# Kernel optimization log

Measured on AMD Instinct MI355X. Metric: run time of the kernel, lower is better.

## Reference

```python
import jax, jax.numpy as jnp
import numpy as np
import math

B, T, C = 4, 2048, 768
H = 12
D = C // H  # head dim 64

def setup_inputs() -> dict:
    key = jax.random.key(0)
    ks = jax.random.split(key, 7)
    hidden_states = jax.random.normal(ks[0], (B, T, C), dtype=jnp.float32)
    attention_mask = jnp.ones((B, T), dtype=jnp.float32)
    # torch nn.Linear weights are [out, in]; y = x @ W.T + b
    s = 1.0 / math.sqrt(C)
    Wq = jax.random.uniform(ks[1], (C, C), jnp.float32, -s, s)
    bq = jax.random.uniform(ks[2], (C,), jnp.float32, -s, s)
    Wk = jax.random.uniform(ks[3], (C, C), jnp.float32, -s, s)
    bk = jax.random.uniform(ks[4], (C,), jnp.float32, -s, s)
    Wv = jax.random.uniform(ks[5], (C, C), jnp.float32, -s, s)
    bv = jax.random.uniform(ks[6], (C,), jnp.float32, -s, s)
    return {"hidden_states": hidden_states, "attention_mask": attention_mask,
            "Wq": Wq, "bq": bq, "Wk": Wk, "bk": bk, "Wv": Wv, "bv": bv}

def _split_heads(x):
    # [B,T,C] -> [B,H,T,D]
    b, t, c = x.shape
    return x.reshape(b, t, H, D).transpose(0, 2, 1, 3)

def reference(hidden_states, attention_mask, Wq, bq, Wk, bk, Wv, bv):
    q = _split_heads(hidden_states @ Wq.T + bq)
    k = _split_heads(hidden_states @ Wk.T + bk)
    v = _split_heads(hidden_states @ Wv.T + bv)
    scores = jnp.einsum("bhqd,bhkd->bhqk", q, k) / jnp.sqrt(jnp.float32(D))
    # mask: [B,T] -> additive bias [B,1,1,T]
    bias = (1.0 - attention_mask)[:, None, None, :] * -10000.0
    scores = scores + bias
    probs = jax.nn.softmax(scores, axis=-1)  # dropout prob = 0 -> identity
    ctx = jnp.einsum("bhqk,bhkd->bhqd", probs, v)
    # [B,H,T,D] -> [B,T,C]
    return ctx.transpose(0, 2, 1, 3).reshape(hidden_states.shape[0], hidden_states.shape[1], C)
```

## Files before the change

### kernel.cpp

```cpp
#include <hip/hip_runtime.h>
#include <hip/hip_bf16.h>
#include <cstdint>

#define DI __device__ __forceinline__

constexpr int Bz = 4, Tz = 2048, Cz = 768, Hz = 12, Dz = 64;
constexpr float QSCALE = 0.18033688011112042f;

typedef __attribute__((ext_vector_type(4))) float f32x4;
typedef __attribute__((ext_vector_type(16))) float f32x16;
typedef __attribute__((ext_vector_type(8))) __bf16 bf16x8;
typedef __attribute__((ext_vector_type(4))) __bf16 bf16x4;
typedef __attribute__((ext_vector_type(2))) __bf16 bf16x2;

typedef __attribute__((address_space(1))) void gvoid;
typedef __attribute__((address_space(3))) void lvoid;

DI void gload16(const void* g, void* l) {
  __builtin_amdgcn_global_load_lds((gvoid*)g, (lvoid*)l, 16, 0, 0);
}

DI f32x4 mfma16(bf16x8 a, bf16x8 b, f32x4 c) {
  return __builtin_amdgcn_mfma_f32_16x16x32_bf16(a, b, c, 0, 0, 0);
}
DI f32x16 mfma32(bf16x8 a, bf16x8 b, f32x16 c) {
  return __builtin_amdgcn_mfma_f32_32x32x16_bf16(a, b, c, 0, 0, 0);
}

DI uint32_t pk2(float a, float b) {
  bf16x2 t;
  t[0] = (__bf16)a;
  t[1] = (__bf16)b;
  return __builtin_bit_cast(uint32_t, t);
}

union FragU { bf16x8 v; uint32_t u[4]; };

__global__ void cvt_all_k(const float* __restrict__ x,
                          const float* __restrict__ wq, const float* __restrict__ wk,
                          const float* __restrict__ wv, __bf16* __restrict__ Xb,
                          __bf16* __restrict__ Wb) {
  int i = blockIdx.x * blockDim.x + threadIdx.x;
  const float* s;
  __bf16* d;
  int r;
  if (i < 1572864) {
    s = x; d = Xb; r = i;
  } else {
    int j = i - 1572864;
    const int which = j / 147456;
    r = j - which * 147456;
    s = (which == 0) ? wq : (which == 1) ? wk : wv;
    d = Wb + which * 589824 * 2;
    d = Wb + which * 589824;
  }
  const float4 v = reinterpret_cast<const float4*>(s)[r];
  bf16x4 o = {(__bf16)v.x, (__bf16)v.y, (__bf16)v.z, (__bf16)v.w};
  reinterpret_cast<bf16x4*>(d)[r] = o;
}

__global__ __launch_bounds__(256, 4) void qkv_gemm_k(
    const __bf16* __restrict__ Xb, const __bf16* __restrict__ Wb,
    const float* __restrict__ bq, const float* __restrict__ bk,
    const float* __restrict__ bv, __bf16* __restrict__ Qo,
    __bf16* __restrict__ Ko, __bf16* __restrict__ Vo) {
  __shared__ __align__(16) __bf16 As[128 * 64];
  __shared__ __align__(16) __bf16 Bs[128 * 64];

  const int tid = threadIdx.x;
  const int lane = tid & 63;
  const int w = tid >> 6;
  const int wr = w >> 1, wc = w & 1;
  const int g = lane >> 4, lr = lane & 15;

  const int wgid = (blockIdx.x & 7) * 144 + (blockIdx.x >> 3);
  const int tn = wgid % 18, tm = wgid / 18;
  const int m0 = tm * 128, n0 = tn * 128;

  f32x4 acc[4][4] = {};

  for (int kt = 0; kt < Cz; kt += 64) {
#pragma unroll
    for (int rep = 0; rep < 4; ++rep) {
      const int c = rep * 256 + tid;
      const int row = c >> 3, blk = c & 7;
      const int col = ((blk ^ (row & 7)) << 3);
      gload16(&Xb[(size_t)(m0 + row) * Cz + kt + col], &As[c << 3]);
      gload16(&Wb[(size_t)(n0 + row) * Cz + kt + col], &Bs[c << 3]);
    }
    __syncthreads();
#pragma unroll
    for (int kk = 0; kk < 2; ++kk) {
      bf16x8 a[4], b[4];
#pragma unroll
      for (int m = 0; m < 4; ++m) {
        const int row = wr * 64 + m * 16 + lr;
        a[m] = *reinterpret_cast<const bf16x8*>(
            &As[row * 64 + (((kk * 4 + g) ^ (row & 7)) << 3)]);
      }
#pragma unroll
      for (int n = 0; n < 4; ++n) {
        const int row = wc * 64 + n * 16 + lr;
        b[n] = *reinterpret_cast<const bf16x8*>(
            &Bs[row * 64 + (((kk * 4 + g) ^ (row & 7)) << 3)]);
      }
      __builtin_amdgcn_s_setprio(1);
#pragma unroll
      for (int m = 0; m < 4; ++m)
#pragma unroll
        for (int n = 0; n < 4; ++n) acc[m][n] = mfma16(a[m], b[n], acc[m][n]);
      __builtin_amdgcn_s_setprio(0);
    }
    __syncthreads();
  }

  const int bb = m0 >> 11;
  const int tbase = m0 & 2047;
  if (tn >= 12) {
#pragma unroll
    for (int n = 0; n < 4; ++n) {
      const int cc = (n0 - 1536) + wc * 64 + n * 16 + lr;
      const int h = cc >> 6, d = cc & 63;
      const float bsv = bv[cc];
      const int bh = bb * Hz + h;
#pragma unroll
      for (int m = 0; m < 4; ++m) {
        const int tloc = tbase + wr * 64 + m * 16 + g * 4;
        const int k16 = tloc >> 4;
        bf16x4 pkv;
#pragma unroll
        for (int j = 0; j < 4; ++j) pkv[j] = (__bf16)(acc[m][n][j] + bsv);
        *reinterpret_cast<bf16x4*>(
            &Vo[((size_t)(bh * 128 + k16) * 64 + d) * 16 + (tloc & 15)]) = pkv;
      }
    }
  } else {
    const bool isQ = (tn < 6);
#pragma unroll
    for (int n = 0; n < 4; ++n) {
      const int gn = n0 + wc * 64 + n * 16 + lr;
      const int cc = isQ ? gn : (gn - 768);
      const int h = cc >> 6, d = cc & 63;
      const float bsv = isQ ? bq[cc] : bk[cc];
      __bf16* dst = isQ ? Qo : Ko;
      const int bh = bb * Hz + h;
#pragma unroll
      for (int m = 0; m < 4; ++m) {
#pragma unroll
        for (int j = 0; j < 4; ++j) {
          const int t = tbase + wr * 64 + m * 16 + g * 4 + j;
          float v = acc[m][n][j] + bsv;
          if (isQ) v *= QSCALE;
          dst[(size_t)(bh * Tz + t) * Dz + d] = (__bf16)v;
        }
      }
    }
  }
}

__global__ __launch_bounds__(256, 3) void attn_k(
    const __bf16* __restrict__ Qg, const __bf16* __restrict__ Kg,
    const __bf16* __restrict__ Vc, const float* __restrict__ mask,
    float* __restrict__ out) {
  __shared__ __align__(16) __bf16 Ks[2][4096];

  const int tid = threadIdx.x;
  const int lane = tid & 63;
  const int w = tid >> 6;
  const int hi = lane >> 5;
  const int l31 = lane & 31;

  const int wg = (blockIdx.x & 7) * 96 + (blockIdx.x >> 3);
  const int bh = wg >> 4, qt = wg & 15;
  const int bb = bh / Hz, h = bh - bb * Hz;
  const int q0 = qt * 128 + w * 32;

  const size_t qkbase = (size_t)bh * Tz * Dz;
  const size_t vcb = (size_t)bh * Tz * Dz;
  const float* maskp = &mask[bb * Tz];

  int* flag = (int*)&Ks[1][0];
  if (tid == 0) *flag = 0;
  __syncthreads();
  {
    int mybad = 0;
    for (int i = tid; i < Tz; i += 256) mybad |= (maskp[i] != 1.0f);
    if (__any(mybad) && lane == 0) atomicOr(flag, 1);
  }

#pragma unroll
  for (int rep = 0; rep < 2; ++rep) {
    const int c = rep * 256 + tid;
    const int row = c >> 3, blk = c & 7;
    const int col = ((blk ^ (row & 7)) << 3);
    gload16(&Kg[qkbase + (size_t)row * Dz + col], &Ks[0][c << 3]);
  }

  bf16x8 qB[4];
#pragma unroll
  for (int ks = 0; ks < 4; ++ks)
    qB[ks] = *reinterpret_cast<const bf16x8*>(
        &Qg[qkbase + (size_t)(q0 + l31) * Dz + ks * 16 + hi * 8]);

  __syncthreads();
  const bool use_mask = (*flag != 0);

  int off4[4];
#pragma unroll
  for (int i = 0; i < 4; ++i)
    off4[i] = l31 * 64 + (((i * 2 + hi) ^ (l31 & 7)) << 3);

  const int vlane0 = l31 * 16 + hi * 8;

  f32x16 o0 = {}, o1 = {};
  float lpart = 0.f;

  for (int t2 = 0; t2 < 16; ++t2) {
#pragma unroll
    for (int sub = 0; sub < 2; ++sub) {
      const int t = 2 * t2 + sub;
      __syncthreads();

      bf16x8 vB[4][2];
#pragma unroll
      for (int ps4 = 0; ps4 < 4; ++ps4) {
        const size_t cb = vcb + (size_t)(t * 4 + ps4) * 1024;
        vB[ps4][0] = *reinterpret_cast<const bf16x8*>(&Vc[cb + vlane0]);
        vB[ps4][1] = *reinterpret_cast<const bf16x8*>(&Vc[cb + 512 + vlane0]);
      }

      if (t < 31) {
        const int kt1 = (t + 1) * 64;
#pragma unroll
        for (int rep = 0; rep < 2; ++rep) {
          const int c = rep * 256 + tid;
          const int row = c >> 3, blk = c & 7;
          const int col = ((blk ^ (row & 7)) << 3);
          gload16(&Kg[qkbase + (size_t)(kt1 + row) * Dz + col],
                  &Ks[sub ^ 1][c << 3]);
        }
      }
      const int kt = t * 64;

#pragma unroll
      for (int kblk = 0; kblk < 2; ++kblk) {
        bf16x8 kA[4];
#pragma unroll
        for (int ks = 0; ks < 4; ++ks)
          kA[ks] = *reinterpret_cast<const bf16x8*>(
              &Ks[sub][kblk * 2048 + off4[ks]]);

        f32x16 s = {};
        __builtin_amdgcn_s_setprio(1);
#pragma unroll
        for (int ks = 0; ks < 4; ++ks) s = mfma32(kA[ks], qB[ks], s);
        __builtin_amdgcn_s_setprio(0);

        float p[16];
        if (use_mask) {
#pragma unroll
          for (int r = 0; r < 16; ++r) {
            const int kg = kt + kblk * 32 + (r & 3) + 8 * (r >> 2) + 4 * hi;
            p[r] = __builtin_amdgcn_exp2f(
                s[r] + (1.0f - maskp[kg]) * -14426.950408889634f);
            lpart += p[r];
          }
        } else {
#pragma unroll
          for (int r = 0; r < 16; ++r) {
            p[r] = __builtin_amdgcn_exp2f(s[r]);
            lpart += p[r];
          }
        }

        uint32_t a0 = pk2(p[0], p[1]), a1 = pk2(p[4], p[5]);
        uint32_t a2 = pk2(p[8], p[9]), a3 = pk2(p[12], p[13]);
        uint32_t b0 = pk2(p[2], p[3]), b1 = pk2(p[6], p[7]);
        uint32_t b2 = pk2(p[10], p[11]), b3 = pk2(p[14], p[15]);
        asm volatile("v_permlane32_swap_b32 %0, %1" : "+v"(a0), "+v"(a1));
        asm volatile("v_permlane32_swap_b32 %0, %1" : "+v"(b0), "+v"(b1));
        asm volatile("v_permlane32_swap_b32 %0, %1" : "+v"(a2), "+v"(a3));
        asm volatile("v_permlane32_swap_b32 %0, %1" : "+v"(b2), "+v"(b3));
        FragU pf0, pf1;
        pf0.u[0] = a0; pf0.u[1] = b0; pf0.u[2] = a1; pf0.u[3] = b1;
        pf1.u[0] = a2; pf1.u[1] = b2; pf1.u[2] = a3; pf1.u[3] = b3;

        __builtin_amdgcn_s_setprio(1);
        o0 = mfma32(pf0.v, vB[kblk * 2][0], o0);
        o1 = mfma32(pf0.v, vB[kblk * 2][1], o1);
        o0 = mfma32(pf1.v, vB[kblk * 2 + 1][0], o0);
        o1 = mfma32(pf1.v, vB[kblk * 2 + 1][1], o1);
        __builtin_amdgcn_s_setprio(0);
      }
    }
  }

  float lfin = lpart + __shfl_xor(lpart, 32);
  const float inv = 1.0f / lfin;
#pragma unroll
  for (int r = 0; r < 16; ++r) {
    const int qr = (r & 3) + 8 * (r >> 2) + 4 * hi;
    const float invr = __shfl(inv, qr);
    float* orow = &out[(size_t)(bb * Tz + q0 + qr) * Cz + h * Dz + l31];
    orow[0] = o0[r] * invr;
    orow[32] = o1[r] * invr;
  }
}

extern "C" void kernel_launch(void* const* d_in, const int* in_sizes, int n_in,
                              void* d_out, int out_size, void* d_ws,
                              size_t ws_size, hipStream_t stream) {
  const float* x = (const float*)d_in[0];
  const float* mask = (const float*)d_in[1];
  const float* Wq = (const float*)d_in[2];
  const float* bq = (const float*)d_in[3];
  const float* Wk = (const float*)d_in[4];
  const float* bk = (const float*)d_in[5];
  const float* Wv = (const float*)d_in[6];
  const float* bv = (const float*)d_in[7];
  float* out = (float*)d_out;

  char* ws = (char*)d_ws;
  __bf16* Xb = (__bf16*)ws;
  __bf16* Wb = (__bf16*)(ws + 12582912);
  __bf16* Qb = (__bf16*)(ws + 16131072);
  __bf16* Kb = (__bf16*)(ws + 16131072 + 12582912);
  __bf16* Vb = (__bf16*)(ws + 16131072 + 2 * 12582912);

  cvt_all_k<<<7872, 256, 0, stream>>>(x, Wq, Wk, Wv, Xb, Wb);
  qkv_gemm_k<<<1152, 256, 0, stream>>>(Xb, Wb, bq, bk, bv, Qb, Kb, Vb);
  attn_k<<<768, 256, 0, stream>>>(Qb, Kb, Vb, mask, out);
}
```

Measured before the change: 116.4 us.

## Split attention key range across two wave groups with LDS reduction

Each attention workgroup now has 512 threads, with two groups of four waves. Each group processes half of the key sequence for the same 128 query rows, and the partial outputs and row sums are combined through LDS at the end. The goal is to double wave-level parallelism and halve the serial key loop per wave, hiding more latency. In exchange it needs more LDS for the doubled K buffers, extra barriers and a reduction step. It also changes the K swizzle pattern, splits the row-sum accumulator into two to shorten the dependency chain, and removes a dead store in the convert kernel.

```diff
diff --git a/kernel.cpp b/kernel.cpp
--- a/kernel.cpp
+++ b/kernel.cpp
@@ -35,6 +35,8 @@
 }
 
 union FragU { bf16x8 v; uint32_t u[4]; };
+
+DI int kswz(int row) { return (row & 7) ^ (((row >> 3) & 3) << 1); }
 
 __global__ void cvt_all_k(const float* __restrict__ x,
                           const float* __restrict__ wq, const float* __restrict__ wk,
@@ -51,7 +53,6 @@
     const int which = j / 147456;
     r = j - which * 147456;
     s = (which == 0) ? wq : (which == 1) ? wk : wv;
-    d = Wb + which * 589824 * 2;
     d = Wb + which * 589824;
   }
   const float4 v = reinterpret_cast<const float4*>(s)[r];
@@ -158,42 +159,44 @@
   }
 }
 
-__global__ __launch_bounds__(256, 3) void attn_k(
+__global__ __launch_bounds__(512, 6) void attn_k(
     const __bf16* __restrict__ Qg, const __bf16* __restrict__ Kg,
     const __bf16* __restrict__ Vc, const float* __restrict__ mask,
     float* __restrict__ out) {
-  __shared__ __align__(16) __bf16 Ks[2][4096];
+  __shared__ __align__(16) __bf16 KsAll[2][2][4096];
+  __shared__ int flag;
 
   const int tid = threadIdx.x;
   const int lane = tid & 63;
   const int w = tid >> 6;
+  const int w4 = w & 3;
+  const int gw = w >> 2;
   const int hi = lane >> 5;
   const int l31 = lane & 31;
 
   const int wg = (blockIdx.x & 7) * 96 + (blockIdx.x >> 3);
   const int bh = wg >> 4, qt = wg & 15;
   const int bb = bh / Hz, h = bh - bb * Hz;
-  const int q0 = qt * 128 + w * 32;
+  const int q0 = qt * 128 + w4 * 32;
+  const int kb0 = gw * 1024;
 
   const size_t qkbase = (size_t)bh * Tz * Dz;
-  const size_t vcb = (size_t)bh * Tz * Dz;
   const float* maskp = &mask[bb * Tz];
 
-  int* flag = (int*)&Ks[1][0];
-  if (tid == 0) *flag = 0;
+  if (tid == 0) flag = 0;
   __syncthreads();
   {
     int mybad = 0;
-    for (int i = tid; i < Tz; i += 256) mybad |= (maskp[i] != 1.0f);
-    if (__any(mybad) && lane == 0) atomicOr(flag, 1);
-  }
-
-#pragma unroll
-  for (int rep = 0; rep < 2; ++rep) {
-    const int c = rep * 256 + tid;
+    for (int i = tid; i < Tz; i += 512) mybad |= (maskp[i] != 1.0f);
+    if (__any(mybad) && lane == 0) atomicOr(&flag, 1);
+  }
+
+  {
+    const int c = tid;
     const int row = c >> 3, blk = c & 7;
-    const int col = ((blk ^ (row & 7)) << 3);
-    gload16(&Kg[qkbase + (size_t)row * Dz + col], &Ks[0][c << 3]);
+    const int col = ((blk ^ kswz(row)) << 3);
+    gload16(&Kg[qkbase + (size_t)row * Dz + col], &KsAll[0][0][c << 3]);
+    gload16(&Kg[qkbase + (size_t)(1024 + row) * Dz + col], &KsAll[1][0][c << 3]);
   }
 
   bf16x8 qB[4];
@@ -203,19 +206,22 @@
         &Qg[qkbase + (size_t)(q0 + l31) * Dz + ks * 16 + hi * 8]);
 
   __syncthreads();
-  const bool use_mask = (*flag != 0);
-
+  const bool use_mask = (flag != 0);
+
+  const int f31 = (l31 & 7) ^ (((l31 >> 3) & 3) << 1);
+  const __bf16* ksBase = &KsAll[gw][0][0];
   int off4[4];
 #pragma unroll
   for (int i = 0; i < 4; ++i)
-    off4[i] = l31 * 64 + (((i * 2 + hi) ^ (l31 & 7)) << 3);
+    off4[i] = l31 * 64 + (((i * 2 + hi) ^ f31) << 3);
 
   const int vlane0 = l31 * 16 + hi * 8;
+  const size_t vcb0 = qkbase + (size_t)kb0 * Dz;
 
   f32x16 o0 = {}, o1 = {};
-  float lpart = 0.f;
-
-  for (int t2 = 0; t2 < 16; ++t2) {
+  float lpA = 0.f, lpB = 0.f;
+
+  for (int t2 = 0; t2 < 8; ++t2) {
 #pragma unroll
     for (int sub = 0; sub < 2; ++sub) {
       const int t = 2 * t2 + sub;
@@ -224,23 +230,22 @@
       bf16x8 vB[4][2];
 #pragma unroll
       for (int ps4 = 0; ps4 < 4; ++ps4) {
-        const size_t cb = vcb + (size_t)(t * 4 + ps4) * 1024;
+        const size_t cb = vcb0 + (size_t)(t * 4 + ps4) * 1024;
         vB[ps4][0] = *reinterpret_cast<const bf16x8*>(&Vc[cb + vlane0]);
         vB[ps4][1] = *reinterpret_cast<const bf16x8*>(&Vc[cb + 512 + vlane0]);
       }
 
-      if (t < 31) {
+      if (t < 15) {
         const int kt1 = (t + 1) * 64;
-#pragma unroll
-        for (int rep = 0; rep < 2; ++rep) {
-          const int c = rep * 256 + tid;
-          const int row = c >> 3, blk = c & 7;
-          const int col = ((blk ^ (row & 7)) << 3);
-          gload16(&Kg[qkbase + (size_t)(kt1 + row) * Dz + col],
-                  &Ks[sub ^ 1][c << 3]);
-        }
-      }
-      const int kt = t * 64;
+        const int c = tid;
+        const int row = c >> 3, blk = c & 7;
+        const int col = ((blk ^ kswz(row)) << 3);
+        gload16(&Kg[qkbase + (size_t)(kt1 + row) * Dz + col],
+                &KsAll[0][sub ^ 1][c << 3]);
+        gload16(&Kg[qkbase + (size_t)(1024 + kt1 + row) * Dz + col],
+                &KsAll[1][sub ^ 1][c << 3]);
+      }
+      const int kt = kb0 + t * 64;
 
 #pragma unroll
       for (int kblk = 0; kblk < 2; ++kblk) {
@@ -248,7 +253,7 @@
 #pragma unroll
         for (int ks = 0; ks < 4; ++ks)
           kA[ks] = *reinterpret_cast<const bf16x8*>(
-              &Ks[sub][kblk * 2048 + off4[ks]]);
+              &ksBase[sub * 4096 + kblk * 2048 + off4[ks]]);
 
         f32x16 s = {};
         __builtin_amdgcn_s_setprio(1);
@@ -263,13 +268,13 @@
             const int kg = kt + kblk * 32 + (r & 3) + 8 * (r >> 2) + 4 * hi;
             p[r] = __builtin_amdgcn_exp2f(
                 s[r] + (1.0f - maskp[kg]) * -14426.950408889634f);
-            lpart += p[r];
+            ((r & 1) ? lpB : lpA) += p[r];
           }
         } else {
 #pragma unroll
           for (int r = 0; r < 16; ++r) {
             p[r] = __builtin_amdgcn_exp2f(s[r]);
-            lpart += p[r];
+            ((r & 1) ? lpB : lpA) += p[r];
           }
         }
 
@@ -295,15 +300,38 @@
     }
   }
 
-  float lfin = lpart + __shfl_xor(lpart, 32);
-  const float inv = 1.0f / lfin;
-#pragma unroll
-  for (int r = 0; r < 16; ++r) {
-    const int qr = (r & 3) + 8 * (r >> 2) + 4 * hi;
-    const float invr = __shfl(inv, qr);
-    float* orow = &out[(size_t)(bb * Tz + q0 + qr) * Cz + h * Dz + l31];
-    orow[0] = o0[r] * invr;
-    orow[32] = o1[r] * invr;
+  float* cb = (float*)&KsAll[0][0][0];
+  float lp = lpA + lpB;
+  __syncthreads();
+  if (gw == 1)
+#pragma unroll
+    for (int j = 0; j < 16; ++j) cb[w4 * 1024 + lane * 16 + j] = o0[j];
+  __syncthreads();
+  if (gw == 0)
+#pragma unroll
+    for (int j = 0; j < 16; ++j) o0[j] += cb[w4 * 1024 + lane * 16 + j];
+  __syncthreads();
+  if (gw == 1) {
+#pragma unroll
+    for (int j = 0; j < 16; ++j) cb[w4 * 1024 + lane * 16 + j] = o1[j];
+    cb[4096 + w4 * 64 + lane] = lp;
+  }
+  __syncthreads();
+  if (gw == 0) {
+#pragma unroll
+    for (int j = 0; j < 16; ++j) o1[j] += cb[w4 * 1024 + lane * 16 + j];
+    lp += cb[4096 + w4 * 64 + lane];
+
+    float lfin = lp + __shfl_xor(lp, 32);
+    const float inv = 1.0f / lfin;
+#pragma unroll
+    for (int r = 0; r < 16; ++r) {
+      const int qr = (r & 3) + 8 * (r >> 2) + 4 * hi;
+      const float invr = __shfl(inv, qr);
+      float* orow = &out[(size_t)(bb * Tz + q0 + qr) * Cz + h * Dz + l31];
+      orow[0] = o0[r] * invr;
+      orow[32] = o1[r] * invr;
+    }
   }
 }
 
@@ -329,5 +357,5 @@
 
   cvt_all_k<<<7872, 256, 0, stream>>>(x, Wq, Wk, Wv, Xb, Wb);
   qkv_gemm_k<<<1152, 256, 0, stream>>>(Xb, Wb, bq, bk, bv, Qb, Kb, Vb);
-  attn_k<<<768, 256, 0, stream>>>(Qb, Kb, Vb, mask, out);
-}
+  attn_k<<<768, 512, 0, stream>>>(Qb, Kb, Vb, mask, out);
+}
```

Measured after the change: 446.1 us. 283% more time.

## Deepen K prefetch to four LDS buffers with partial waitcnt barrier

Applied to the files above, without the earlier changes.

Makes the attention kernel's K staging a 4-slot LDS ring with prefetch distance two, so each global_load_lds has more time to land. In the unmasked path it replaces the full __syncthreads with s_waitcnt vmcnt(2) plus a raw barrier, so the newest prefetch can stay in flight. It also templates the loop on the mask flag, splits the row-sum into two accumulators, and raises launch bounds to 4 waves/SIMD. The hand-written vmcnt assumes a fixed count of outstanding vector loads per iteration; if the compiler reorders loads, the sync could be wrong.

```diff
diff --git a/kernel.cpp b/kernel.cpp
--- a/kernel.cpp
+++ b/kernel.cpp
@@ -51,7 +51,6 @@
     const int which = j / 147456;
     r = j - which * 147456;
     s = (which == 0) ? wq : (which == 1) ? wk : wv;
-    d = Wb + which * 589824 * 2;
     d = Wb + which * 589824;
   }
   const float4 v = reinterpret_cast<const float4*>(s)[r];
@@ -158,87 +157,33 @@
   }
 }
 
-__global__ __launch_bounds__(256, 3) void attn_k(
-    const __bf16* __restrict__ Qg, const __bf16* __restrict__ Kg,
-    const __bf16* __restrict__ Vc, const float* __restrict__ mask,
-    float* __restrict__ out) {
-  __shared__ __align__(16) __bf16 Ks[2][4096];
-
-  const int tid = threadIdx.x;
-  const int lane = tid & 63;
-  const int w = tid >> 6;
-  const int hi = lane >> 5;
-  const int l31 = lane & 31;
-
-  const int wg = (blockIdx.x & 7) * 96 + (blockIdx.x >> 3);
-  const int bh = wg >> 4, qt = wg & 15;
-  const int bb = bh / Hz, h = bh - bb * Hz;
-  const int q0 = qt * 128 + w * 32;
-
-  const size_t qkbase = (size_t)bh * Tz * Dz;
-  const size_t vcb = (size_t)bh * Tz * Dz;
-  const float* maskp = &mask[bb * Tz];
-
-  int* flag = (int*)&Ks[1][0];
-  if (tid == 0) *flag = 0;
-  __syncthreads();
-  {
-    int mybad = 0;
-    for (int i = tid; i < Tz; i += 256) mybad |= (maskp[i] != 1.0f);
-    if (__any(mybad) && lane == 0) atomicOr(flag, 1);
-  }
-
-#pragma unroll
-  for (int rep = 0; rep < 2; ++rep) {
-    const int c = rep * 256 + tid;
-    const int row = c >> 3, blk = c & 7;
-    const int col = ((blk ^ (row & 7)) << 3);
-    gload16(&Kg[qkbase + (size_t)row * Dz + col], &Ks[0][c << 3]);
-  }
-
-  bf16x8 qB[4];
-#pragma unroll
-  for (int ks = 0; ks < 4; ++ks)
-    qB[ks] = *reinterpret_cast<const bf16x8*>(
-        &Qg[qkbase + (size_t)(q0 + l31) * Dz + ks * 16 + hi * 8]);
-
-  __syncthreads();
-  const bool use_mask = (*flag != 0);
-
-  int off4[4];
-#pragma unroll
-  for (int i = 0; i < 4; ++i)
-    off4[i] = l31 * 64 + (((i * 2 + hi) ^ (l31 & 7)) << 3);
-
-  const int vlane0 = l31 * 16 + hi * 8;
-
-  f32x16 o0 = {}, o1 = {};
-  float lpart = 0.f;
-
-  for (int t2 = 0; t2 < 16; ++t2) {
-#pragma unroll
-    for (int sub = 0; sub < 2; ++sub) {
-      const int t = 2 * t2 + sub;
-      __syncthreads();
-
-      bf16x8 vB[4][2];
-#pragma unroll
-      for (int ps4 = 0; ps4 < 4; ++ps4) {
-        const size_t cb = vcb + (size_t)(t * 4 + ps4) * 1024;
-        vB[ps4][0] = *reinterpret_cast<const bf16x8*>(&Vc[cb + vlane0]);
-        vB[ps4][1] = *reinterpret_cast<const bf16x8*>(&Vc[cb + 512 + vlane0]);
-      }
-
-      if (t < 31) {
-        const int kt1 = (t + 1) * 64;
+template <bool MASKED>
+DI void attn_main(__bf16 (*Ks)[4096], const __bf16* __restrict__ Kg,
+                  const __bf16* __restrict__ Vc, const float* maskp,
+                  size_t qkbase, size_t vcb0, const bf16x8* qB,
+                  const int* off4, int vlane0, int tid, int hi,
+                  f32x16& o0, f32x16& o1, float& lpA, float& lpB) {
+  for (int t4 = 0; t4 < 8; ++t4) {
+#pragma unroll
+    for (int sub = 0; sub < 4; ++sub) {
+      const int t = 4 * t4 + sub;
+      if (t < 30) {
+        const int kt2 = (t + 2) * 64;
 #pragma unroll
         for (int rep = 0; rep < 2; ++rep) {
           const int c = rep * 256 + tid;
           const int row = c >> 3, blk = c & 7;
           const int col = ((blk ^ (row & 7)) << 3);
-          gload16(&Kg[qkbase + (size_t)(kt1 + row) * Dz + col],
-                  &Ks[sub ^ 1][c << 3]);
+          gload16(&Kg[qkbase + (size_t)(kt2 + row) * Dz + col],
+                  &Ks[(sub + 2) & 3][c << 3]);
         }
+      }
+      bf16x8 vB[4][2];
+#pragma unroll
+      for (int ps4 = 0; ps4 < 4; ++ps4) {
+        const size_t cb = vcb0 + (size_t)(t * 4 + ps4) * 1024;
+        vB[ps4][0] = *reinterpret_cast<const bf16x8*>(&Vc[cb + vlane0]);
+        vB[ps4][1] = *reinterpret_cast<const bf16x8*>(&Vc[cb + 512 + vlane0]);
       }
       const int kt = t * 64;
 
@@ -257,20 +202,15 @@
         __builtin_amdgcn_s_setprio(0);
 
         float p[16];
-        if (use_mask) {
-#pragma unroll
-          for (int r = 0; r < 16; ++r) {
+#pragma unroll
+        for (int r = 0; r < 16; ++r) {
+          float sc = s[r];
+          if (MASKED) {
             const int kg = kt + kblk * 32 + (r & 3) + 8 * (r >> 2) + 4 * hi;
-            p[r] = __builtin_amdgcn_exp2f(
-                s[r] + (1.0f - maskp[kg]) * -14426.950408889634f);
-            lpart += p[r];
+            sc += (1.0f - maskp[kg]) * -14426.950408889634f;
           }
-        } else {
-#pragma unroll
-          for (int r = 0; r < 16; ++r) {
-            p[r] = __builtin_amdgcn_exp2f(s[r]);
-            lpart += p[r];
-          }
+          p[r] = __builtin_amdgcn_exp2f(sc);
+          ((r & 1) ? lpB : lpA) += p[r];
         }
 
         uint32_t a0 = pk2(p[0], p[1]), a1 = pk2(p[4], p[5]);
@@ -292,10 +232,89 @@
         o1 = mfma32(pf1.v, vB[kblk * 2 + 1][1], o1);
         __builtin_amdgcn_s_setprio(0);
       }
-    }
-  }
-
-  float lfin = lpart + __shfl_xor(lpart, 32);
+
+      if (MASKED) {
+        __syncthreads();
+      } else {
+        __builtin_amdgcn_sched_barrier(0);
+        asm volatile("s_waitcnt vmcnt(2)" ::: "memory");
+        __builtin_amdgcn_s_barrier();
+        __builtin_amdgcn_sched_barrier(0);
+      }
+    }
+  }
+}
+
+__global__ __launch_bounds__(256, 4) void attn_k(
+    const __bf16* __restrict__ Qg, const __bf16* __restrict__ Kg,
+    const __bf16* __restrict__ Vc, const float* __restrict__ mask,
+    float* __restrict__ out) {
+  __shared__ __align__(16) __bf16 Ks[4][4096];
+  __shared__ int flag;
+
+  const int tid = threadIdx.x;
+  const int lane = tid & 63;
+  const int w = tid >> 6;
+  const int hi = lane >> 5;
+  const int l31 = lane & 31;
+
+  const int wg = (blockIdx.x & 7) * 96 + (blockIdx.x >> 3);
+  const int bh = wg >> 4, qt = wg & 15;
+  const int bb = bh / Hz, h = bh - bb * Hz;
+  const int q0 = qt * 128 + w * 32;
+
+  const size_t qkbase = (size_t)bh * Tz * Dz;
+  const float* maskp = &mask[bb * Tz];
+
+  if (tid == 0) flag = 0;
+  __syncthreads();
+  {
+    int mybad = 0;
+    for (int i = tid; i < Tz; i += 256) mybad |= (maskp[i] != 1.0f);
+    if (__any(mybad) && lane == 0) atomicOr(&flag, 1);
+  }
+
+#pragma unroll
+  for (int tt = 0; tt < 2; ++tt) {
+#pragma unroll
+    for (int rep = 0; rep < 2; ++rep) {
+      const int c = rep * 256 + tid;
+      const int row = c >> 3, blk = c & 7;
+      const int col = ((blk ^ (row & 7)) << 3);
+      gload16(&Kg[qkbase + (size_t)(tt * 64 + row) * Dz + col],
+              &Ks[tt][c << 3]);
+    }
+  }
+
+  bf16x8 qB[4];
+#pragma unroll
+  for (int ks = 0; ks < 4; ++ks)
+    qB[ks] = *reinterpret_cast<const bf16x8*>(
+        &Qg[qkbase + (size_t)(q0 + l31) * Dz + ks * 16 + hi * 8]);
+
+  __syncthreads();
+  const bool use_mask = (flag != 0);
+
+  int off4[4];
+#pragma unroll
+  for (int i = 0; i < 4; ++i)
+    off4[i] = l31 * 64 + (((i * 2 + hi) ^ (l31 & 7)) << 3);
+
+  const int vlane0 = l31 * 16 + hi * 8;
+  const size_t vcb0 = qkbase;
+
+  f32x16 o0 = {}, o1 = {};
+  float lpA = 0.f, lpB = 0.f;
+
+  if (use_mask)
+    attn_main<true>(Ks, Kg, Vc, maskp, qkbase, vcb0, qB, off4, vlane0, tid,
+                    hi, o0, o1, lpA, lpB);
+  else
+    attn_main<false>(Ks, Kg, Vc, maskp, qkbase, vcb0, qB, off4, vlane0, tid,
+                     hi, o0, o1, lpA, lpB);
+
+  float lp = lpA + lpB;
+  float lfin = lp + __shfl_xor(lp, 32);
   const float inv = 1.0f / lfin;
 #pragma unroll
   for (int r = 0; r < 16; ++r) {
```

Measured after the change: 252.5 us. 2.17x slower.
